# Kernel optimization log

Hardware: AMD Instinct MI355X
Metric: run time of the kernel (lower is better)

## Reference

```python
import jax, jax.numpy as jnp
import numpy as np

N = 524288
BASIS_RES = (32, 64, 128, 256)
CHANNELS = (4, 4, 4, 4)
FREQS = (1.0, 2.0, 4.0, 8.0)
COEF_RES = 64
L = 4
HID = 128
IN_FEAT = sum(CHANNELS)  # 16


def trilerp(grid, pts):
    """grid: [C, D, H, W]; pts: [N, 3] (x,y,z) in [-1,1]. align_corners=True trilinear
    gather, matching torch.nn.functional.grid_sample semantics. Returns [N, C]."""
    C, D, H, W = grid.shape
    sizes = jnp.asarray([W, H, D], dtype=pts.dtype)
    c = (pts + 1.0) * 0.5 * (sizes - 1.0)          # pixel coords [N,3]
    c0 = jnp.floor(c)
    f = c - c0                                      # fractional part [N,3]
    fx, fy, fz = f[:, 0], f[:, 1], f[:, 2]
    x0 = jnp.clip(c0[:, 0].astype(jnp.int32), 0, W - 1)
    y0 = jnp.clip(c0[:, 1].astype(jnp.int32), 0, H - 1)
    z0 = jnp.clip(c0[:, 2].astype(jnp.int32), 0, D - 1)
    x1 = jnp.minimum(x0 + 1, W - 1)
    y1 = jnp.minimum(y0 + 1, H - 1)
    z1 = jnp.minimum(z0 + 1, D - 1)
    g = lambda zi, yi, xi: grid[:, zi, yi, xi]      # [C, N]
    v = (g(z0, y0, x0) * (1 - fz) * (1 - fy) * (1 - fx)
         + g(z0, y0, x1) * (1 - fz) * (1 - fy) * fx
         + g(z0, y1, x0) * (1 - fz) * fy * (1 - fx)
         + g(z0, y1, x1) * (1 - fz) * fy * fx
         + g(z1, y0, x0) * fz * (1 - fy) * (1 - fx)
         + g(z1, y0, x1) * fz * (1 - fy) * fx
         + g(z1, y1, x0) * fz * fy * (1 - fx)
         + g(z1, y1, x1) * fz * fy * fx)
    return v.T                                      # [N, C]


def setup_inputs() -> dict:
    key = jax.random.key(0)
    ks = jax.random.split(key, 20)
    inp = {"x": jax.random.uniform(ks[0], (N, 3), jnp.float32) * 2.0 - 1.0}
    for i, (r, c) in enumerate(zip(BASIS_RES, CHANNELS)):
        inp[f"g{i}"] = jax.random.uniform(ks[1 + i], (c, r, r, r), jnp.float32)
    inp["coef_grid"] = jax.random.uniform(ks[5], (L, COEF_RES, COEF_RES, COEF_RES), jnp.float32)
    dims = [IN_FEAT] + [HID] * 6 + [HID]            # 7 linear layers
    for j in range(7):
        din, dout = dims[j], dims[j + 1]
        inp[f"W{j}"] = jax.random.normal(ks[6 + j], (din, dout), jnp.float32) * (1.0 / np.sqrt(din))
        inp[f"B{j}"] = jnp.zeros((dout,), jnp.float32)
    return inp


def reference(x, g0, g1, g2, g3, coef_grid,
              W0, B0, W1, B1, W2, B2, W3, B3, W4, B4, W5, B5, W6, B6):
    coefs = trilerp(coef_grid, x)                   # [N, L]
    feats = []
    for i, g in enumerate((g0, g1, g2, g3)):
        enc = 2.0 * ((FREQS[i] * x) % 1.0) - 1.0    # sawtooth encoding in [-1,1)
        feats.append(trilerp(g, enc) * coefs[:, i:i + 1])
    h = jnp.concatenate(feats, -1)                  # [N, sum(channels)]
    # dropout(p=0.01) in eval mode: identity
    Ws = [(W0, B0), (W1, B1), (W2, B2), (W3, B3), (W4, B4), (W5, B5), (W6, B6)]
    for W, B in Ws[:-1]:
        h = jax.nn.relu(h @ W + B)
    W, B = Ws[-1]
    return h @ W + B                                # [N, HID]
```

## Files before the change

### kernel.cpp

```cpp
#include <hip/hip_runtime.h>
#include <hip/hip_fp16.h>

#define N_PTS 524288

typedef __attribute__((ext_vector_type(8))) short bf16x8;
typedef __attribute__((ext_vector_type(4))) short bf16x4;
typedef __attribute__((ext_vector_type(4))) float f32x4;

__device__ __forceinline__ unsigned short f2bf(float f) {
    unsigned u = __builtin_bit_cast(unsigned, f);
    u = (u + 0x7FFFu + ((u >> 16) & 1u)) >> 16;
    return (unsigned short)u;
}

__device__ __forceinline__ float encf(float v, float f) {
    float t = v * f;
    return 2.0f * (t - floorf(t)) - 1.0f;
}

template <int R>
__global__ __launch_bounds__(256) void ileaveh_kernel(const float* __restrict__ g,
                                                      unsigned short* __restrict__ gi) {
    constexpr int V = R * R * R;
    int idx = blockIdx.x * 256 + threadIdx.x;
    ushort4 v;
    v.x = __half_as_ushort(__float2half(g[idx]));
    v.y = __half_as_ushort(__float2half(g[idx + V]));
    v.z = __half_as_ushort(__float2half(g[idx + 2 * V]));
    v.w = __half_as_ushort(__float2half(g[idx + 3 * V]));
    *(ushort4*)(&gi[(size_t)idx * 4]) = v;
}

__device__ __forceinline__ float4 h4f(const unsigned short* p) {
    uint2 u = *(const uint2*)p;
    float4 r;
    r.x = __half2float(__ushort_as_half((unsigned short)(u.x & 0xffffu)));
    r.y = __half2float(__ushort_as_half((unsigned short)(u.x >> 16)));
    r.z = __half2float(__ushort_as_half((unsigned short)(u.y & 0xffffu)));
    r.w = __half2float(__ushort_as_half((unsigned short)(u.y >> 16)));
    return r;
}

template <int R>
__device__ __forceinline__ float4 trilerp4h(const unsigned short* __restrict__ gi,
                                            float px, float py, float pz) {
    constexpr float S = 0.5f * (float)(R - 1);
    float cx = (px + 1.0f) * S;
    float cy = (py + 1.0f) * S;
    float cz = (pz + 1.0f) * S;
    float fx0 = floorf(cx), fy0 = floorf(cy), fz0 = floorf(cz);
    float fx = cx - fx0, fy = cy - fy0, fz = cz - fz0;
    int ix0 = min(max((int)fx0, 0), R - 1);
    int iy0 = min(max((int)fy0, 0), R - 1);
    int iz0 = min(max((int)fz0, 0), R - 1);
    int dx = (ix0 < R - 1) ? 4 : 0;
    int dy = (iy0 < R - 1) ? 4 * R : 0;
    int dz = (iz0 < R - 1) ? 4 * R * R : 0;
    const unsigned short* p = gi + 4 * ((size_t)iz0 * (R * R) + iy0 * R + ix0);

    float4 v000 = h4f(p);
    float4 v001 = h4f(p + dx);
    float4 v010 = h4f(p + dy);
    float4 v011 = h4f(p + dy + dx);
    float4 v100 = h4f(p + dz);
    float4 v101 = h4f(p + dz + dx);
    float4 v110 = h4f(p + dz + dy);
    float4 v111 = h4f(p + dz + dy + dx);

    float gx0 = 1.0f - fx, gy0 = 1.0f - fy, gz0 = 1.0f - fz;
    float w00 = gz0 * gy0, w01 = gz0 * fy, w10 = fz * gy0, w11 = fz * fy;
    float w000 = w00 * gx0, w001 = w00 * fx;
    float w010 = w01 * gx0, w011 = w01 * fx;
    float w100 = w10 * gx0, w101 = w10 * fx;
    float w110 = w11 * gx0, w111 = w11 * fx;

    float4 r;
    r.x = v000.x * w000 + v001.x * w001 + v010.x * w010 + v011.x * w011 +
          v100.x * w100 + v101.x * w101 + v110.x * w110 + v111.x * w111;
    r.y = v000.y * w000 + v001.y * w001 + v010.y * w010 + v011.y * w011 +
          v100.y * w100 + v101.y * w101 + v110.y * w110 + v111.y * w111;
    r.z = v000.z * w000 + v001.z * w001 + v010.z * w010 + v011.z * w011 +
          v100.z * w100 + v101.z * w101 + v110.z * w110 + v111.z * w111;
    r.w = v000.w * w000 + v001.w * w001 + v010.w * w010 + v011.w * w011 +
          v100.w * w100 + v101.w * w101 + v110.w * w110 + v111.w * w111;
    return r;
}

template <int R>
__device__ __forceinline__ float4 trilerp4s(const float* __restrict__ g,
                                            float px, float py, float pz) {
    constexpr float S = 0.5f * (float)(R - 1);
    float cx = (px + 1.0f) * S;
    float cy = (py + 1.0f) * S;
    float cz = (pz + 1.0f) * S;
    float fx0 = floorf(cx), fy0 = floorf(cy), fz0 = floorf(cz);
    float fx = cx - fx0, fy = cy - fy0, fz = cz - fz0;
    int ix0 = min(max((int)fx0, 0), R - 1);
    int iy0 = min(max((int)fy0, 0), R - 1);
    int iz0 = min(max((int)fz0, 0), R - 1);
    int dx = (ix0 < R - 1) ? 1 : 0;
    int dy = (iy0 < R - 1) ? R : 0;
    int dz = (iz0 < R - 1) ? R * R : 0;
    int base = iz0 * (R * R) + iy0 * R + ix0;

    float gx0 = 1.0f - fx, gy0 = 1.0f - fy, gz0 = 1.0f - fz;
    float w00 = gz0 * gy0, w01 = gz0 * fy, w10 = fz * gy0, w11 = fz * fy;
    float w000 = w00 * gx0, w001 = w00 * fx;
    float w010 = w01 * gx0, w011 = w01 * fx;
    float w100 = w10 * gx0, w101 = w10 * fx;
    float w110 = w11 * gx0, w111 = w11 * fx;

    float4 out;
    float r[4];
#pragma unroll
    for (int c = 0; c < 4; ++c) {
        const float* gc = g + (size_t)c * (R * R * R);
        r[c] = gc[base] * w000 + gc[base + dx] * w001 + gc[base + dy] * w010 +
               gc[base + dy + dx] * w011 + gc[base + dz] * w100 +
               gc[base + dz + dx] * w101 + gc[base + dz + dy] * w110 +
               gc[base + dz + dy + dx] * w111;
    }
    out.x = r[0]; out.y = r[1]; out.z = r[2]; out.w = r[3];
    return out;
}

__global__ __launch_bounds__(256) void feat_i_kernel(
    const float* __restrict__ x,
    const unsigned short* __restrict__ g0i, const unsigned short* __restrict__ g1i,
    const unsigned short* __restrict__ g2i, const unsigned short* __restrict__ g3i,
    const unsigned short* __restrict__ coefi,
    unsigned short* __restrict__ feats) {
    int i = blockIdx.x * 256 + threadIdx.x;
    float px = x[3 * i + 0], py = x[3 * i + 1], pz = x[3 * i + 2];

    float4 cf = trilerp4h<64>(coefi, px, py, pz);
    float4 t0 = trilerp4h<32>(g0i, encf(px, 1.f), encf(py, 1.f), encf(pz, 1.f));
    float4 t1 = trilerp4h<64>(g1i, encf(px, 2.f), encf(py, 2.f), encf(pz, 2.f));
    float4 t2 = trilerp4h<128>(g2i, encf(px, 4.f), encf(py, 4.f), encf(pz, 4.f));
    float4 t3 = trilerp4h<256>(g3i, encf(px, 8.f), encf(py, 8.f), encf(pz, 8.f));

    float o[16];
    o[0] = t0.x * cf.x; o[1] = t0.y * cf.x; o[2] = t0.z * cf.x; o[3] = t0.w * cf.x;
    o[4] = t1.x * cf.y; o[5] = t1.y * cf.y; o[6] = t1.z * cf.y; o[7] = t1.w * cf.y;
    o[8] = t2.x * cf.z; o[9] = t2.y * cf.z; o[10] = t2.z * cf.z; o[11] = t2.w * cf.z;
    o[12] = t3.x * cf.w; o[13] = t3.y * cf.w; o[14] = t3.z * cf.w; o[15] = t3.w * cf.w;

    bf16x8 lo, hi;
#pragma unroll
    for (int j = 0; j < 8; ++j) {
        lo[j] = (short)f2bf(o[j]);
        hi[j] = (short)f2bf(o[8 + j]);
    }
    bf16x8* dst = (bf16x8*)(feats + (size_t)i * 16);
    dst[0] = lo;
    dst[1] = hi;
}

__global__ __launch_bounds__(256) void feat_s_kernel(
    const float* __restrict__ x,
    const float* __restrict__ g0, const float* __restrict__ g1,
    const float* __restrict__ g2, const float* __restrict__ g3,
    const float* __restrict__ coef,
    unsigned short* __restrict__ feats) {
    int i = blockIdx.x * 256 + threadIdx.x;
    float px = x[3 * i + 0], py = x[3 * i + 1], pz = x[3 * i + 2];

    float4 cf = trilerp4s<64>(coef, px, py, pz);
    float4 t0 = trilerp4s<32>(g0, encf(px, 1.f), encf(py, 1.f), encf(pz, 1.f));
    float4 t1 = trilerp4s<64>(g1, encf(px, 2.f), encf(py, 2.f), encf(pz, 2.f));
    float4 t2 = trilerp4s<128>(g2, encf(px, 4.f), encf(py, 4.f), encf(pz, 4.f));
    float4 t3 = trilerp4s<256>(g3, encf(px, 8.f), encf(py, 8.f), encf(pz, 8.f));

    float o[16];
    o[0] = t0.x * cf.x; o[1] = t0.y * cf.x; o[2] = t0.z * cf.x; o[3] = t0.w * cf.x;
    o[4] = t1.x * cf.y; o[5] = t1.y * cf.y; o[6] = t1.z * cf.y; o[7] = t1.w * cf.y;
    o[8] = t2.x * cf.z; o[9] = t2.y * cf.z; o[10] = t2.z * cf.z; o[11] = t2.w * cf.z;
    o[12] = t3.x * cf.w; o[13] = t3.y * cf.w; o[14] = t3.z * cf.w; o[15] = t3.w * cf.w;

    bf16x8 lo, hi;
#pragma unroll
    for (int j = 0; j < 8; ++j) {
        lo[j] = (short)f2bf(o[j]);
        hi[j] = (short)f2bf(o[8 + j]);
    }
    bf16x8* dst = (bf16x8*)(feats + (size_t)i * 16);
    dst[0] = lo;
    dst[1] = hi;
}

__global__ __launch_bounds__(256) void prep_kernel(
    const float* __restrict__ W0, const float* __restrict__ W1,
    const float* __restrict__ W2, const float* __restrict__ W3,
    const float* __restrict__ W4, const float* __restrict__ W5,
    const float* __restrict__ W6,
    const float* __restrict__ B0, const float* __restrict__ B1,
    const float* __restrict__ B2, const float* __restrict__ B3,
    const float* __restrict__ B4, const float* __restrict__ B5,
    const float* __restrict__ B6,
    unsigned short* __restrict__ wt, float* __restrict__ biases) {
    int tid = blockIdx.x * 256 + threadIdx.x;
    if (tid < 102400) {
        int l, e;
        if (tid < 4096) { l = 0; e = tid; }
        else { l = 1 + (tid - 4096) / 16384; e = (tid - 4096) & 16383; }
        int j = e & 7;
        int lane = (e >> 3) & 63;
        int ni = (e >> 9) & 7;
        int kk = (e >> 12) & 3;
        int lr = lane & 15;
        int q = lane >> 4;
        int n = ni * 16 + lr;
        const float* W = (l == 0) ? W0 : (l == 1) ? W1 : (l == 2) ? W2
                        : (l == 3) ? W3 : (l == 4) ? W4 : (l == 5) ? W5 : W6;
        float v;
        if (l == 0) {
            int k = q * 8 + j;
            v = (k < 16) ? W[k * 128 + n] : 0.0f;
        } else {
            int h = (2 * kk + (j >> 2)) * 16 + q * 4 + (j & 3);
            v = W[h * 128 + n];
        }
        wt[tid] = f2bf(v);
    } else if (tid < 102400 + 896) {
        int e = tid - 102400;
        int l = e >> 7;
        const float* B = (l == 0) ? B0 : (l == 1) ? B1 : (l == 2) ? B2
                        : (l == 3) ? B3 : (l == 4) ? B4 : (l == 5) ? B5 : B6;
        biases[e] = B[e & 127];
    }
}

#define WBUF 16640

__device__ __forceinline__ void stage16(const unsigned short* __restrict__ gsrc,
                                        unsigned short* lbase) {
    __builtin_amdgcn_global_load_lds(
        (const __attribute__((address_space(1))) void*)gsrc,
        (__attribute__((address_space(3))) void*)lbase, 16, 0, 0);
}

__global__ __launch_bounds__(256, 2) void mlp_kernel(
    const unsigned short* __restrict__ feats,
    const unsigned short* __restrict__ wt,
    const float* __restrict__ biases,
    float* __restrict__ out) {
    __shared__ __attribute__((aligned(16))) unsigned short Wlds[2 * WBUF];

    const int t = threadIdx.x;
    const int lane = t & 63;
    const int w = t >> 6;
    const int lr = lane & 15;
    const int q = lane >> 4;
    const size_t rowq = (size_t)blockIdx.x * 256 + w * 64;

    {
#pragma unroll
        for (int i = 0; i < 2; ++i) {
            int idx = i * 4 + w;
            stage16(wt + idx * 512 + lane * 8, Wlds + idx * 512);
        }
        if (t < 128) ((float*)(Wlds + 16384))[t] = biases[t];
    }

    bf16x8 h0[4];
#pragma unroll
    for (int mi = 0; mi < 4; ++mi) {
        if (q < 2)
            h0[mi] = *(const bf16x8*)(feats + (rowq + mi * 16 + lr) * 16 + q * 8);
        else
            h0[mi] = (bf16x8)0;
    }
    __syncthreads();

    f32x4 acc[4][8];

    {
        const unsigned short* w1 = wt + 4096;
#pragma unroll
        for (int i = 0; i < 8; ++i) {
            int idx = i * 4 + w;
            stage16(w1 + idx * 512 + lane * 8, Wlds + WBUF + idx * 512);
        }
        if (t < 128) ((float*)(Wlds + WBUF + 16384))[t] = biases[128 + t];

        const unsigned short* cw = Wlds;
        const float* cb = (const float*)(Wlds + 16384);
#pragma unroll
        for (int ni = 0; ni < 8; ++ni) {
            f32x4 bv = *(const f32x4*)(cb + ni * 16 + q * 4);
#pragma unroll
            for (int mi = 0; mi < 4; ++mi) acc[mi][ni] = bv;
        }
#pragma unroll
        for (int ni = 0; ni < 8; ++ni) {
            bf16x8 wf = *(const bf16x8*)(cw + (ni * 64 + lane) * 8);
#pragma unroll
            for (int mi = 0; mi < 4; ++mi)
                acc[mi][ni] = __builtin_amdgcn_mfma_f32_16x16x32_bf16(
                    wf, h0[mi], acc[mi][ni], 0, 0, 0);
        }
        __syncthreads();
    }

    bf16x8 hf[4][4];
    for (int l = 1; l < 7; ++l) {
        unsigned short* cwm = Wlds + (l & 1) * WBUF;
        if (l < 6) {
            const unsigned short* wn = wt + 4096 + l * 16384;
            unsigned short* nb = Wlds + ((l + 1) & 1) * WBUF;
#pragma unroll
            for (int i = 0; i < 8; ++i) {
                int idx = i * 4 + w;
                stage16(wn + idx * 512 + lane * 8, nb + idx * 512);
            }
            if (t < 128) ((float*)(nb + 16384))[t] = biases[(l + 1) * 128 + t];
        }

#pragma unroll
        for (int mi = 0; mi < 4; ++mi)
#pragma unroll
            for (int kk = 0; kk < 4; ++kk) {
                bf16x8 v;
#pragma unroll
                for (int jp = 0; jp < 8; ++jp)
                    v[jp] = (short)f2bf(fmaxf(acc[mi][2 * kk + (jp >> 2)][jp & 3], 0.0f));
                hf[mi][kk] = v;
            }
        const float* cb = (const float*)(cwm + 16384);
#pragma unroll
        for (int ni = 0; ni < 8; ++ni) {
            f32x4 bv = *(const f32x4*)(cb + ni * 16 + q * 4);
#pragma unroll
            for (int mi = 0; mi < 4; ++mi) acc[mi][ni] = bv;
        }
#pragma unroll
        for (int kk = 0; kk < 4; ++kk) {
            bf16x8 wf[8];
#pragma unroll
            for (int ni = 0; ni < 8; ++ni)
                wf[ni] = *(const bf16x8*)(cwm + ((kk * 8 + ni) * 64 + lane) * 8);
#pragma unroll
            for (int ni = 0; ni < 8; ++ni)
#pragma unroll
                for (int mi = 0; mi < 4; ++mi)
                    acc[mi][ni] = __builtin_amdgcn_mfma_f32_16x16x32_bf16(
                        wf[ni], hf[mi][kk], acc[mi][ni], 0, 0, 0);
        }
        if (l < 6) __syncthreads();
    }

#pragma unroll
    for (int mi = 0; mi < 4; ++mi)
#pragma unroll
        for (int ni = 0; ni < 8; ++ni) {
            *(f32x4*)(&out[(rowq + mi * 16 + lr) * 128 + ni * 16 + q * 4]) =
                acc[mi][ni];
        }
}

extern "C" void kernel_launch(void* const* d_in, const int* in_sizes, int n_in,
                              void* d_out, int out_size, void* d_ws, size_t ws_size,
                              hipStream_t stream) {
    const float* x = (const float*)d_in[0];
    const float* g0 = (const float*)d_in[1];
    const float* g1 = (const float*)d_in[2];
    const float* g2 = (const float*)d_in[3];
    const float* g3 = (const float*)d_in[4];
    const float* coef = (const float*)d_in[5];
    const float* W[7];
    const float* B[7];
    for (int j = 0; j < 7; ++j) {
        W[j] = (const float*)d_in[6 + 2 * j];
        B[j] = (const float*)d_in[7 + 2 * j];
    }

    char* ws = (char*)d_ws;
    unsigned short* feats = (unsigned short*)ws;
    unsigned short* wt = (unsigned short*)(ws + 16777216);
    float* biases = (float*)(ws + 16982016);
    unsigned short* coefi = (unsigned short*)(ws + 16985600);
    unsigned short* g0i = (unsigned short*)(ws + 19082752);
    unsigned short* g1i = (unsigned short*)(ws + 19344896);
    unsigned short* g2i = (unsigned short*)(ws + 21442048);
    unsigned short* g3i = (unsigned short*)d_out;

    prep_kernel<<<404, 256, 0, stream>>>(W[0], W[1], W[2], W[3], W[4], W[5], W[6],
                                         B[0], B[1], B[2], B[3], B[4], B[5], B[6],
                                         wt, biases);

    bool fast = ws_size >= 38219264ull;
    if (fast) {
        ileaveh_kernel<64><<<1024, 256, 0, stream>>>(coef, coefi);
        ileaveh_kernel<32><<<128, 256, 0, stream>>>(g0, g0i);
        ileaveh_kernel<64><<<1024, 256, 0, stream>>>(g1, g1i);
        ileaveh_kernel<128><<<8192, 256, 0, stream>>>(g2, g2i);
        ileaveh_kernel<256><<<65536, 256, 0, stream>>>(g3, g3i);
        feat_i_kernel<<<N_PTS / 256, 256, 0, stream>>>(x, g0i, g1i, g2i, g3i,
                                                       coefi, feats);
    } else {
        feat_s_kernel<<<N_PTS / 256, 256, 0, stream>>>(x, g0, g1, g2, g3, coef,
                                                       feats);
    }

    mlp_kernel<<<N_PTS / 256, 256, 0, stream>>>(feats, wt, biases, (float*)d_out);
}
```

Measured before the change: 773.3 us.

## Bucket-sort points by finest-grid cell to improve gather locality

Adds a counting sort of the input points into 1024 spatial buckets keyed on their cell in the 256^3 sawtooth-encoded grid, using histogram, scan and scatter kernels. Feature extraction then runs on the sorted points so neighbouring threads gather from nearby grid cells, which should cut cache misses on the large grid. The MLP reads features back through an inverse permutation so the output stays in the original order. The cost is four extra kernels, global atomics, and scattered 32-byte feature reads in the MLP. This path is only taken when the workspace is large enough.

```diff
diff --git a/kernel.cpp b/kernel.cpp
--- a/kernel.cpp
+++ b/kernel.cpp
@@ -2,6 +2,7 @@
 #include <hip/hip_fp16.h>
 
 #define N_PTS 524288
+#define NBUCK 1024
 
 typedef __attribute__((ext_vector_type(8))) short bf16x8;
 typedef __attribute__((ext_vector_type(4))) short bf16x4;
@@ -16,6 +17,63 @@
 __device__ __forceinline__ float encf(float v, float f) {
     float t = v * f;
     return 2.0f * (t - floorf(t)) - 1.0f;
+}
+
+__device__ __forceinline__ int bucket_of(float px, float py, float pz) {
+    float cx = (encf(px, 8.f) + 1.0f) * 127.5f;
+    float cy = (encf(py, 8.f) + 1.0f) * 127.5f;
+    float cz = (encf(pz, 8.f) + 1.0f) * 127.5f;
+    int ix = min(max((int)floorf(cx), 0), 255);
+    int iy = min(max((int)floorf(cy), 0), 255);
+    int iz = min(max((int)floorf(cz), 0), 255);
+    return ((iz >> 4) << 6) | ((iy >> 5) << 3) | (ix >> 5);
+}
+
+__global__ __launch_bounds__(1024) void zero_hist_kernel(unsigned* __restrict__ hist) {
+    hist[threadIdx.x] = 0u;
+}
+
+__global__ __launch_bounds__(256) void hist_kernel(const float* __restrict__ x,
+                                                   unsigned* __restrict__ hist) {
+    __shared__ unsigned lh[NBUCK];
+    int t = threadIdx.x;
+    for (int i = t; i < NBUCK; i += 256) lh[i] = 0u;
+    __syncthreads();
+    int gid = blockIdx.x * 256 + t;
+    atomicAdd(&lh[bucket_of(x[3 * gid], x[3 * gid + 1], x[3 * gid + 2])], 1u);
+    __syncthreads();
+    for (int i = t; i < NBUCK; i += 256) {
+        unsigned c = lh[i];
+        if (c) atomicAdd(&hist[i], c);
+    }
+}
+
+__global__ __launch_bounds__(1024) void scan_kernel(const unsigned* __restrict__ hist,
+                                                    unsigned* __restrict__ cursor) {
+    __shared__ unsigned s[NBUCK];
+    int t = threadIdx.x;
+    unsigned mine = hist[t];
+    s[t] = mine;
+    __syncthreads();
+    for (int off = 1; off < NBUCK; off <<= 1) {
+        unsigned v = (t >= off) ? s[t - off] : 0u;
+        __syncthreads();
+        s[t] += v;
+        __syncthreads();
+    }
+    cursor[t] = s[t] - mine;
+}
+
+__global__ __launch_bounds__(256) void scatter_kernel(const float* __restrict__ x,
+                                                      unsigned* __restrict__ cursor,
+                                                      float4* __restrict__ rec,
+                                                      int* __restrict__ invPos) {
+    int gid = blockIdx.x * 256 + threadIdx.x;
+    float px = x[3 * gid], py = x[3 * gid + 1], pz = x[3 * gid + 2];
+    int b = bucket_of(px, py, pz);
+    unsigned pos = atomicAdd(&cursor[b], 1u);
+    rec[pos] = make_float4(px, py, pz, 0.0f);
+    invPos[gid] = (int)pos;
 }
 
 template <int R>
@@ -124,6 +182,46 @@
     return out;
 }
 
+__device__ __forceinline__ void feat_core(
+    float px, float py, float pz,
+    const unsigned short* __restrict__ g0i, const unsigned short* __restrict__ g1i,
+    const unsigned short* __restrict__ g2i, const unsigned short* __restrict__ g3i,
+    const unsigned short* __restrict__ coefi,
+    unsigned short* __restrict__ feats, size_t i) {
+    float4 cf = trilerp4h<64>(coefi, px, py, pz);
+    float4 t0 = trilerp4h<32>(g0i, encf(px, 1.f), encf(py, 1.f), encf(pz, 1.f));
+    float4 t1 = trilerp4h<64>(g1i, encf(px, 2.f), encf(py, 2.f), encf(pz, 2.f));
+    float4 t2 = trilerp4h<128>(g2i, encf(px, 4.f), encf(py, 4.f), encf(pz, 4.f));
+    float4 t3 = trilerp4h<256>(g3i, encf(px, 8.f), encf(py, 8.f), encf(pz, 8.f));
+
+    float o[16];
+    o[0] = t0.x * cf.x; o[1] = t0.y * cf.x; o[2] = t0.z * cf.x; o[3] = t0.w * cf.x;
+    o[4] = t1.x * cf.y; o[5] = t1.y * cf.y; o[6] = t1.z * cf.y; o[7] = t1.w * cf.y;
+    o[8] = t2.x * cf.z; o[9] = t2.y * cf.z; o[10] = t2.z * cf.z; o[11] = t2.w * cf.z;
+    o[12] = t3.x * cf.w; o[13] = t3.y * cf.w; o[14] = t3.z * cf.w; o[15] = t3.w * cf.w;
+
+    bf16x8 lo, hi;
+#pragma unroll
+    for (int j = 0; j < 8; ++j) {
+        lo[j] = (short)f2bf(o[j]);
+        hi[j] = (short)f2bf(o[8 + j]);
+    }
+    bf16x8* dst = (bf16x8*)(feats + i * 16);
+    dst[0] = lo;
+    dst[1] = hi;
+}
+
+__global__ __launch_bounds__(256) void feat_sorted_kernel(
+    const float4* __restrict__ rec,
+    const unsigned short* __restrict__ g0i, const unsigned short* __restrict__ g1i,
+    const unsigned short* __restrict__ g2i, const unsigned short* __restrict__ g3i,
+    const unsigned short* __restrict__ coefi,
+    unsigned short* __restrict__ feats) {
+    int i = blockIdx.x * 256 + threadIdx.x;
+    float4 r = rec[i];
+    feat_core(r.x, r.y, r.z, g0i, g1i, g2i, g3i, coefi, feats, (size_t)i);
+}
+
 __global__ __launch_bounds__(256) void feat_i_kernel(
     const float* __restrict__ x,
     const unsigned short* __restrict__ g0i, const unsigned short* __restrict__ g1i,
@@ -131,29 +229,8 @@
     const unsigned short* __restrict__ coefi,
     unsigned short* __restrict__ feats) {
     int i = blockIdx.x * 256 + threadIdx.x;
-    float px = x[3 * i + 0], py = x[3 * i + 1], pz = x[3 * i + 2];
-
-    float4 cf = trilerp4h<64>(coefi, px, py, pz);
-    float4 t0 = trilerp4h<32>(g0i, encf(px, 1.f), encf(py, 1.f), encf(pz, 1.f));
-    float4 t1 = trilerp4h<64>(g1i, encf(px, 2.f), encf(py, 2.f), encf(pz, 2.f));
-    float4 t2 = trilerp4h<128>(g2i, encf(px, 4.f), encf(py, 4.f), encf(pz, 4.f));
-    float4 t3 = trilerp4h<256>(g3i, encf(px, 8.f), encf(py, 8.f), encf(pz, 8.f));
-
-    float o[16];
-    o[0] = t0.x * cf.x; o[1] = t0.y * cf.x; o[2] = t0.z * cf.x; o[3] = t0.w * cf.x;
-    o[4] = t1.x * cf.y; o[5] = t1.y * cf.y; o[6] = t1.z * cf.y; o[7] = t1.w * cf.y;
-    o[8] = t2.x * cf.z; o[9] = t2.y * cf.z; o[10] = t2.z * cf.z; o[11] = t2.w * cf.z;
-    o[12] = t3.x * cf.w; o[13] = t3.y * cf.w; o[14] = t3.z * cf.w; o[15] = t3.w * cf.w;
-
-    bf16x8 lo, hi;
-#pragma unroll
-    for (int j = 0; j < 8; ++j) {
-        lo[j] = (short)f2bf(o[j]);
-        hi[j] = (short)f2bf(o[8 + j]);
-    }
-    bf16x8* dst = (bf16x8*)(feats + (size_t)i * 16);
-    dst[0] = lo;
-    dst[1] = hi;
+    feat_core(x[3 * i], x[3 * i + 1], x[3 * i + 2], g0i, g1i, g2i, g3i, coefi,
+              feats, (size_t)i);
 }
 
 __global__ __launch_bounds__(256) void feat_s_kernel(
@@ -241,6 +318,7 @@
 
 __global__ __launch_bounds__(256, 2) void mlp_kernel(
     const unsigned short* __restrict__ feats,
+    const int* __restrict__ invPos,
     const unsigned short* __restrict__ wt,
     const float* __restrict__ biases,
     float* __restrict__ out) {
@@ -265,8 +343,10 @@
     bf16x8 h0[4];
 #pragma unroll
     for (int mi = 0; mi < 4; ++mi) {
+        size_t r = rowq + mi * 16 + lr;
+        size_t p = invPos ? (size_t)invPos[r] : r;
         if (q < 2)
-            h0[mi] = *(const bf16x8*)(feats + (rowq + mi * 16 + lr) * 16 + q * 8);
+            h0[mi] = *(const bf16x8*)(feats + p * 16 + q * 8);
         else
             h0[mi] = (bf16x8)0;
     }
@@ -382,6 +462,10 @@
     unsigned short* g0i = (unsigned short*)(ws + 19082752);
     unsigned short* g1i = (unsigned short*)(ws + 19344896);
     unsigned short* g2i = (unsigned short*)(ws + 21442048);
+    unsigned* hist = (unsigned*)(ws + 38219264);
+    unsigned* cursor = (unsigned*)(ws + 38223360);
+    float4* rec = (float4*)(ws + 38227456);
+    int* invPos = (int*)(ws + 46616064);
     unsigned short* g3i = (unsigned short*)d_out;
 
     prep_kernel<<<404, 256, 0, stream>>>(W[0], W[1], W[2], W[3], W[4], W[5], W[6],
@@ -389,18 +473,32 @@
                                          wt, biases);
 
     bool fast = ws_size >= 38219264ull;
+    bool fast2 = ws_size >= 48713216ull;
     if (fast) {
         ileaveh_kernel<64><<<1024, 256, 0, stream>>>(coef, coefi);
         ileaveh_kernel<32><<<128, 256, 0, stream>>>(g0, g0i);
         ileaveh_kernel<64><<<1024, 256, 0, stream>>>(g1, g1i);
         ileaveh_kernel<128><<<8192, 256, 0, stream>>>(g2, g2i);
         ileaveh_kernel<256><<<65536, 256, 0, stream>>>(g3, g3i);
-        feat_i_kernel<<<N_PTS / 256, 256, 0, stream>>>(x, g0i, g1i, g2i, g3i,
-                                                       coefi, feats);
+        if (fast2) {
+            zero_hist_kernel<<<1, 1024, 0, stream>>>(hist);
+            hist_kernel<<<N_PTS / 256, 256, 0, stream>>>(x, hist);
+            scan_kernel<<<1, 1024, 0, stream>>>(hist, cursor);
+            scatter_kernel<<<N_PTS / 256, 256, 0, stream>>>(x, cursor, rec, invPos);
+            feat_sorted_kernel<<<N_PTS / 256, 256, 0, stream>>>(rec, g0i, g1i, g2i,
+                                                                g3i, coefi, feats);
+            mlp_kernel<<<N_PTS / 256, 256, 0, stream>>>(feats, invPos, wt, biases,
+                                                        (float*)d_out);
+        } else {
+            feat_i_kernel<<<N_PTS / 256, 256, 0, stream>>>(x, g0i, g1i, g2i, g3i,
+                                                           coefi, feats);
+            mlp_kernel<<<N_PTS / 256, 256, 0, stream>>>(feats, nullptr, wt, biases,
+                                                        (float*)d_out);
+        }
     } else {
         feat_s_kernel<<<N_PTS / 256, 256, 0, stream>>>(x, g0, g1, g2, g3, coef,
                                                        feats);
-    }
-
-    mlp_kernel<<<N_PTS / 256, 256, 0, stream>>>(feats, wt, biases, (float*)d_out);
-}
+        mlp_kernel<<<N_PTS / 256, 256, 0, stream>>>(feats, nullptr, wt, biases,
+                                                    (float*)d_out);
+    }
+}
```

After: 867.3 us. 12.2% more time.
